# Kernel optimization log

Hardware: AMD Instinct MI355X
Metric: run time of the kernel (lower is better)

The kernel has to match this reference:

```python
import jax, jax.numpy as jnp
import numpy as np


def setup_inputs() -> dict:
    key = jax.random.key(0)
    k1, k2, k3, k4 = jax.random.split(key, 4)
    B, S, H = 1, 2048, 3072
    E, I = 4, 8192  # num_experts, intermediate_size
    x = jax.random.normal(k1, (B, S, H), dtype=jnp.float32)
    gate_w = jax.random.normal(k2, (E, H), dtype=jnp.float32) * 0.02
    w_gate_up = jax.random.normal(k3, (E, 2 * I, H), dtype=jnp.float32) * 0.02
    w_down = jax.random.normal(k4, (E, H, I), dtype=jnp.float32) * 0.02
    return {"x": x, "gate_w": gate_w, "w_gate_up": w_gate_up, "w_down": w_down, "top_k": 2}


def reference(x, gate_w, w_gate_up, w_down, top_k):
    # x: [B, S, H]; gate_w: [E, H]; w_gate_up: [E, 2I, H]; w_down: [E, H, I]
    B, S, H = x.shape
    E = gate_w.shape[0]
    # Gating: softmax over experts, then top-k values/indices
    logits = jnp.einsum('bsh,eh->bse', x, gate_w)
    probs = jax.nn.softmax(logits, axis=-1)
    gate_values, gate_indices = jax.lax.top_k(probs, top_k)  # [B, S, k]
    # Dense all-expert SwiGLU MLP (as in the original module)
    xf = x.reshape(-1, H)                                     # [N, H]
    up_states = jnp.einsum('nh,eih->nei', xf, w_gate_up)      # [N, E, 2I]
    gate, up = jnp.split(up_states, 2, axis=-1)               # [N, E, I] each
    hidden = up * jax.nn.silu(gate)                           # SwiGLU
    expert_out = jnp.einsum('nei,ehi->neh', hidden, w_down)   # [N, E, H]
    expert_out = expert_out.reshape(B, S, E, H)
    # Gather selected experts and combine with gate values
    sel = jnp.take_along_axis(expert_out, gate_indices[..., None], axis=2)  # [B, S, k, H]
    moe_output = jnp.sum(sel * gate_values[..., None], axis=2)              # [B, S, H]
    return moe_output
```

## Files before the change

kernel.cpp:

```cpp
#include <hip/hip_runtime.h>

#define S 2048
#define Hd 3072
#define NE 4
#define Id 8192
#define BK 64
#define RMAX 5120

typedef __attribute__((ext_vector_type(8))) short short8;
typedef __attribute__((ext_vector_type(4))) float f32x4;

__device__ __forceinline__ unsigned short f2bf(float f) {
    unsigned u = __builtin_bit_cast(unsigned, f);
    u += 0x7FFFu + ((u >> 16) & 1u);
    return (unsigned short)(u >> 16);
}

__device__ __forceinline__ void gload_lds16(const void* g, void* l) {
    __builtin_amdgcn_global_load_lds(
        (const __attribute__((address_space(1))) unsigned int*)g,
        (__attribute__((address_space(3))) unsigned int*)l,
        16, 0, 0);
}

#define BAR() __builtin_amdgcn_s_barrier();
#define LGKM0_SB() { asm volatile("s_waitcnt lgkmcnt(0)" ::: "memory"); __builtin_amdgcn_sched_barrier(0); }
#define VM6_SB()  { asm volatile("s_waitcnt vmcnt(6)" ::: "memory"); __builtin_amdgcn_sched_barrier(0); }

__global__ void gate_topk_kernel(const float* __restrict__ x,
                                 const float* __restrict__ gw,
                                 int* __restrict__ tok_e,
                                 float* __restrict__ tok_v) {
    const int t = blockIdx.x;
    const int lane = threadIdx.x & 63;
    const int wave = threadIdx.x >> 6;
    __shared__ float logits[NE];
    const float* xp = x + (size_t)t * Hd;
    const float* wp = gw + (size_t)wave * Hd;
    float s = 0.f;
    for (int h = lane; h < Hd; h += 64) s += xp[h] * wp[h];
#pragma unroll
    for (int o = 32; o > 0; o >>= 1) s += __shfl_xor(s, o);
    if (lane == 0) logits[wave] = s;
    __syncthreads();
    if (threadIdx.x == 0) {
        float m = logits[0];
#pragma unroll
        for (int e = 1; e < NE; e++) m = fmaxf(m, logits[e]);
        float p[NE]; float sum = 0.f;
#pragma unroll
        for (int e = 0; e < NE; e++) { p[e] = expf(logits[e] - m); sum += p[e]; }
        float inv = 1.f / sum;
#pragma unroll
        for (int e = 0; e < NE; e++) p[e] *= inv;
        int e0 = 0; float v0 = p[0];
#pragma unroll
        for (int e = 1; e < NE; e++) if (p[e] > v0) { e0 = e; v0 = p[e]; }
        int e1 = -1; float v1 = -1.f;
#pragma unroll
        for (int e = 0; e < NE; e++) if (e != e0 && p[e] > v1) { e1 = e; v1 = p[e]; }
        tok_e[t * 2] = e0; tok_e[t * 2 + 1] = e1;
        tok_v[t * 2] = v0; tok_v[t * 2 + 1] = v1;
    }
}

__global__ void route_kernel(const int* __restrict__ tok_e, const float* __restrict__ tok_v,
                             int* __restrict__ row_token, float* __restrict__ row_gate,
                             int* __restrict__ offsets) {
    __shared__ int cnt[NE], cur[NE], offs[NE + 1];
    const int tid = threadIdx.x;
    if (tid < NE) { cnt[tid] = 0; cur[tid] = 0; }
    __syncthreads();
    for (int i = tid; i < S * 2; i += 256) atomicAdd(&cnt[tok_e[i]], 1);
    __syncthreads();
    if (tid == 0) {
        int o = 0;
        for (int e = 0; e < NE; e++) { offs[e] = o; o += (cnt[e] + 255) / 256 * 256; }
        offs[NE] = o;
        for (int e = 0; e <= NE; e++) offsets[e] = offs[e];
    }
    __syncthreads();
    for (int r = tid; r < RMAX; r += 256) { row_token[r] = 0; row_gate[r] = 0.f; }
    __syncthreads();
    for (int i = tid; i < S * 2; i += 256) {
        int e = tok_e[i];
        int pos = atomicAdd(&cur[e], 1);
        int r = offs[e] + pos;
        row_token[r] = i >> 1;
        row_gate[r] = tok_v[i];
    }
}

__global__ void cvt_bf16_kernel(const float* __restrict__ src,
                                unsigned short* __restrict__ dst, size_t n16) {
    size_t stride = (size_t)gridDim.x * blockDim.x;
    for (size_t i = (size_t)blockIdx.x * blockDim.x + threadIdx.x; i < n16; i += stride) {
        size_t b = i * 16;
        f32x4 a0 = *(const f32x4*)(src + b);
        f32x4 a1 = *(const f32x4*)(src + b + 4);
        f32x4 a2 = *(const f32x4*)(src + b + 8);
        f32x4 a3 = *(const f32x4*)(src + b + 12);
        union { unsigned short u[8]; short8 v; } o0, o1;
#pragma unroll
        for (int j = 0; j < 4; j++) {
            o0.u[j] = f2bf(a0[j]); o0.u[4 + j] = f2bf(a1[j]);
            o1.u[j] = f2bf(a2[j]); o1.u[4 + j] = f2bf(a3[j]);
        }
        *(short8*)(dst + b) = o0.v;
        *(short8*)(dst + b + 8) = o1.v;
    }
}


#define ST_A0(buf, k) { gload_lds16(aP[0] + (k), &Ald[buf][raD[0]][0]); gload_lds16(aP[1] + (k), &Ald[buf][raD[1]][0]); }
#define ST_A1(buf, k) { gload_lds16(aP[2] + (k), &Ald[buf][raD[2]][0]); gload_lds16(aP[3] + (k), &Ald[buf][raD[3]][0]); }
#define ST_B0(buf, k) { gload_lds16(bP[0] + (k), &Bld[buf][rbD[0]][0]); gload_lds16(bP[1] + (k), &Bld[buf][rbD[1]][0]); }
#define ST_B1(buf, k) { gload_lds16(bP[2] + (k), &Bld[buf][rbD[2]][0]); gload_lds16(bP[3] + (k), &Bld[buf][rbD[3]][0]); }

#define READ_AFL(b) _Pragma("unroll") for (int mi = 0; mi < 4; mi++) _Pragma("unroll") for (int kk = 0; kk < 2; kk++) { \
    int row = wm * 128 + mi * 16 + c16; int slot = ((kk << 2) + c4) ^ l7; \
    afL[mi][kk] = *(const short8*)&Ald[b][row][slot * 8]; }
#define READ_AFH(b) _Pragma("unroll") for (int mi = 0; mi < 4; mi++) _Pragma("unroll") for (int kk = 0; kk < 2; kk++) { \
    int row = wm * 128 + 64 + mi * 16 + c16; int slot = ((kk << 2) + c4) ^ l7; \
    afH[mi][kk] = *(const short8*)&Ald[b][row][slot * 8]; }
#define READ_BFL(b) _Pragma("unroll") for (int n = 0; n < 2; n++) _Pragma("unroll") for (int kk = 0; kk < 2; kk++) { \
    int row = wn * 64 + n * 16 + c16; int slot = ((kk << 2) + c4) ^ l7; \
    bfL[n][kk] = *(const short8*)&Bld[b][row][slot * 8]; }
#define READ_BFH(b) _Pragma("unroll") for (int n = 0; n < 2; n++) _Pragma("unroll") for (int kk = 0; kk < 2; kk++) { \
    int row = wn * 64 + 32 + n * 16 + c16; int slot = ((kk << 2) + c4) ^ l7; \
    bfH[n][kk] = *(const short8*)&Bld[b][row][slot * 8]; }

#define MFMA_Q(AF, BF, MO, NO) _Pragma("unroll") for (int mi = 0; mi < 4; mi++) \
    _Pragma("unroll") for (int n = 0; n < 2; n++) _Pragma("unroll") for (int kk = 0; kk < 2; kk++) \
        acc[mi + MO][n + NO] = __builtin_amdgcn_mfma_f32_16x16x32_bf16(AF[mi][kk], BF[n][kk], acc[mi + MO][n + NO], 0, 0, 0);

#define KTILE_BODY(bR, bW, kN, kNN) { \
    short8 afL[4][2], afH[4][2], bfL[2][2], bfH[2][2]; \
     \
    READ_AFL(bR); READ_BFL(bR); \
    ST_B1(bW, kN); \
    BAR(); LGKM0_SB(); \
    __builtin_amdgcn_s_setprio(1); MFMA_Q(afL, bfL, 0, 0); __builtin_amdgcn_s_setprio(0); \
    BAR(); \
     \
    READ_AFH(bR); \
    ST_A0(bR, kNN); \
    BAR(); LGKM0_SB(); \
    __builtin_amdgcn_s_setprio(1); MFMA_Q(afH, bfL, 4, 0); __builtin_amdgcn_s_setprio(0); \
    BAR(); \
     \
    READ_BFH(bR); \
    ST_B0(bR, kNN); \
    BAR(); LGKM0_SB(); \
    __builtin_amdgcn_s_setprio(1); MFMA_Q(afL, bfH, 0, 2); __builtin_amdgcn_s_setprio(0); \
    BAR(); \
     \
    ST_A1(bR, kNN); \
    BAR(); \
    __builtin_amdgcn_s_setprio(1); MFMA_Q(afH, bfH, 4, 2); __builtin_amdgcn_s_setprio(0); \
    VM6_SB(); BAR(); }

__global__ __launch_bounds__(512, 2)
void gemm1_8p_kernel(const unsigned short* __restrict__ xb,
                     const unsigned short* __restrict__ wgu_b,
                     const int* __restrict__ row_token,
                     const int* __restrict__ offsets,
                     unsigned short* __restrict__ hidden) {
    __shared__ unsigned short Ald[2][256][BK];
    __shared__ unsigned short Bld[2][256][BK];

    const int id = blockIdx.x;
    const int xcd = id & 7, jj = id >> 3;
    const int ct = xcd * 8 + jj / 20;
    const int rt = jj % 20;
    const int rbase = rt * 256;
    if (rbase >= offsets[4]) return;
    int e = 3;
    if (rbase < offsets[1]) e = 0;
    else if (rbase < offsets[2]) e = 1;
    else if (rbase < offsets[3]) e = 2;

    const int tid = threadIdx.x;
    const int l = tid & 63;
    const int w = tid >> 6;
    const int wm = w >> 2, wn = w & 3;
    const int lr = l >> 3;
    const int g8 = ((l & 7) ^ lr) << 3;
    const int c16 = l & 15, c4 = l >> 4, l7 = l & 7;

    const unsigned short* aP[4]; int raD[4];
    const unsigned short* bP[4]; int rbD[4];
#pragma unroll
    for (int j = 0; j < 4; j++) {
        int r0 = w * 8 + (j & 1) * 128 + (j >> 1) * 64;
        raD[j] = r0;
        int tok = row_token[rbase + r0 + lr];
        aP[j] = xb + (size_t)tok * Hd + g8;
        int rb0 = (w & 3) * 8 + (w >> 2) * 64 + (j & 1) * 128 + (j >> 1) * 32;
        rbD[j] = rb0;
        int brow = rb0 + lr;
        int f = brow >> 4;
        size_t wr = (size_t)e * (2 * Id) + (size_t)(f & 1) * Id
                  + (size_t)ct * 128 + ((f >> 1) << 4) + (brow & 15);
        bP[j] = wgu_b + wr * Hd + g8;
    }

    f32x4 acc[8][4];
#pragma unroll
    for (int mi = 0; mi < 8; mi++)
#pragma unroll
        for (int n = 0; n < 4; n++) acc[mi][n] = (f32x4)0.f;

    ST_A0(0, 0); ST_B0(0, 0); ST_A1(0, 0); ST_B1(0, 0);
    ST_A0(1, BK); ST_B0(1, BK); ST_A1(1, BK);
    VM6_SB(); BAR();

    const int nt = Hd / BK;
    for (int t = 0; t < nt; ++t) {
        const int bR = t & 1, bW = bR ^ 1;
        const int kN  = (t + 1 < nt ? t + 1 : nt - 1) * BK;
        const int kNN = (t + 2 < nt ? t + 2 : nt - 1) * BK;
        KTILE_BODY(bR, bW, kN, kNN);
    }
    asm volatile("s_waitcnt vmcnt(0)" ::: "memory");

#pragma unroll
    for (int mi = 0; mi < 8; mi++)
#pragma unroll
        for (int np = 0; np < 2; np++) {
            int col = ct * 128 + (wn * 2 + np) * 16 + c16;
#pragma unroll
            for (int q = 0; q < 4; q++) {
                int row = rbase + wm * 128 + mi * 16 + c4 * 4 + q;
                float gv = acc[mi][2 * np][q], uv = acc[mi][2 * np + 1][q];
                float h = uv * gv / (1.f + expf(-gv));
                hidden[(size_t)row * Id + col] = f2bf(h);
            }
        }
}

__global__ __launch_bounds__(512, 2)
void gemm2_8p_kernel(const unsigned short* __restrict__ hidden,
                     const unsigned short* __restrict__ wd_b,
                     const int* __restrict__ row_token,
                     const float* __restrict__ row_gate,
                     const int* __restrict__ offsets,
                     float* __restrict__ out) {
    __shared__ unsigned short Ald[2][256][BK];
    __shared__ unsigned short Bld[2][256][BK];

    const int rt = blockIdx.x, ct = blockIdx.y;
    const int rbase = rt * 256;
    if (rbase >= offsets[4]) return;
    int e = 3;
    if (rbase < offsets[1]) e = 0;
    else if (rbase < offsets[2]) e = 1;
    else if (rbase < offsets[3]) e = 2;

    const int tid = threadIdx.x;
    const int l = tid & 63;
    const int w = tid >> 6;
    const int wm = w >> 2, wn = w & 3;
    const int lr = l >> 3;
    const int g8 = ((l & 7) ^ lr) << 3;
    const int c16 = l & 15, c4 = l >> 4, l7 = l & 7;

    const unsigned short* aP[4]; int raD[4];
    const unsigned short* bP[4]; int rbD[4];
#pragma unroll
    for (int j = 0; j < 4; j++) {
        int r0 = w * 8 + (j & 1) * 128 + (j >> 1) * 64;
        raD[j] = r0;
        aP[j] = hidden + (size_t)(rbase + r0 + lr) * Id + g8;
        int rb0 = (w & 3) * 8 + (w >> 2) * 64 + (j & 1) * 128 + (j >> 1) * 32;
        rbD[j] = rb0;
        size_t wr = (size_t)e * Hd + (size_t)ct * 256 + rb0 + lr;
        bP[j] = wd_b + wr * Id + g8;
    }

    f32x4 acc[8][4];
#pragma unroll
    for (int mi = 0; mi < 8; mi++)
#pragma unroll
        for (int n = 0; n < 4; n++) acc[mi][n] = (f32x4)0.f;

    ST_A0(0, 0); ST_B0(0, 0); ST_A1(0, 0); ST_B1(0, 0);
    ST_A0(1, BK); ST_B0(1, BK); ST_A1(1, BK);
    VM6_SB(); BAR();

    const int nt = Id / BK;
    for (int t = 0; t < nt; ++t) {
        const int bR = t & 1, bW = bR ^ 1;
        const int kN  = (t + 1 < nt ? t + 1 : nt - 1) * BK;
        const int kNN = (t + 2 < nt ? t + 2 : nt - 1) * BK;
        KTILE_BODY(bR, bW, kN, kNN);
    }
    asm volatile("s_waitcnt vmcnt(0)" ::: "memory");

#pragma unroll
    for (int mi = 0; mi < 8; mi++)
#pragma unroll
        for (int n = 0; n < 4; n++) {
            int col = ct * 256 + wn * 64 + n * 16 + c16;
#pragma unroll
            for (int q = 0; q < 4; q++) {
                int r = rbase + wm * 128 + mi * 16 + c4 * 4 + q;
                int tok = row_token[r];
                float gv = row_gate[r];
                if (gv != 0.f)
                    atomicAdd(&out[(size_t)tok * Hd + col], gv * acc[mi][n][q]);
            }
        }
}


__global__ __launch_bounds__(256, 2)
void gemm1_f32_kernel(const unsigned short* __restrict__ xb,
                      const float* __restrict__ wgu,
                      const int* __restrict__ row_token,
                      const int* __restrict__ offsets,
                      unsigned short* __restrict__ hidden) {
    __shared__ unsigned short As[128][BK];
    __shared__ unsigned short Bg[128][BK];
    __shared__ unsigned short Bu[128][BK];

    const int rt = blockIdx.x, ct = blockIdx.y;
    const int rbase = rt * 128;
    if (rbase >= offsets[4]) return;
    int e = 3;
    if (rbase < offsets[1]) e = 0;
    else if (rbase < offsets[2]) e = 1;
    else if (rbase < offsets[3]) e = 2;

    const int tid = threadIdx.x;
    const int lane = tid & 63;
    const int wave = tid >> 6;
    const int wm = wave >> 1, wn = wave & 1;

    const unsigned short* asrc[4];
#pragma unroll
    for (int i2 = 0; i2 < 4; i2++) {
        int sgi = i2 * 4 + wave;
        int row = sgi * 8 + (lane >> 3);
        int g = (lane & 7) ^ (row & 7);
        int tok = row_token[rbase + row];
        asrc[i2] = xb + (size_t)tok * Hd + g * 8;
    }
    const int col = tid >> 1;
    const int half = tid & 1;
    const size_t grow = (size_t)e * (2 * Id) + (size_t)ct * 128 + col;
    const float* bsrc_g = wgu + grow * Hd + half * 32;
    const float* bsrc_u = wgu + (grow + (size_t)Id) * Hd + half * 32;
    const int csw = col & 7;

    f32x4 accg[4][4], accu[4][4];
#pragma unroll
    for (int m = 0; m < 4; m++)
#pragma unroll
        for (int n = 0; n < 4; n++) { accg[m][n] = (f32x4)0.f; accu[m][n] = (f32x4)0.f; }

    for (int k0 = 0; k0 < Hd; k0 += BK) {
        __syncthreads();
#pragma unroll
        for (int i2 = 0; i2 < 4; i2++) {
            int sgi = i2 * 4 + wave;
            gload_lds16(asrc[i2] + k0, &As[sgi * 8][0]);
        }
        {
            const float* pg = bsrc_g + k0;
            const float* pu = bsrc_u + k0;
            f32x4 vg[8], vu[8];
#pragma unroll
            for (int j = 0; j < 8; j++) vg[j] = *(const f32x4*)(pg + j * 4);
#pragma unroll
            for (int j = 0; j < 8; j++) vu[j] = *(const f32x4*)(pu + j * 4);
#pragma unroll
            for (int j = 0; j < 4; j++) {
                union { unsigned short u[8]; short8 v8; } wg_, wu_;
#pragma unroll
                for (int q = 0; q < 4; q++) {
                    wg_.u[q] = f2bf(vg[2 * j][q]); wg_.u[4 + q] = f2bf(vg[2 * j + 1][q]);
                    wu_.u[q] = f2bf(vu[2 * j][q]); wu_.u[4 + q] = f2bf(vu[2 * j + 1][q]);
                }
                int gs = (half * 4 + j) ^ csw;
                *(short8*)&Bg[col][gs * 8] = wg_.v8;
                *(short8*)&Bu[col][gs * 8] = wu_.v8;
            }
        }
        __syncthreads();
#pragma unroll
        for (int kk = 0; kk < 2; kk++) {
            short8 af[4], bgf[4], buf_[4];
#pragma unroll
            for (int m = 0; m < 4; m++) {
                int r = wm * 64 + m * 16 + (lane & 15);
                int slot = (kk * 4 + (lane >> 4)) ^ (r & 7);
                af[m] = *(const short8*)&As[r][slot * 8];
            }
#pragma unroll
            for (int n = 0; n < 4; n++) {
                int c = wn * 64 + n * 16 + (lane & 15);
                int slot = (kk * 4 + (lane >> 4)) ^ (c & 7);
                bgf[n] = *(const short8*)&Bg[c][slot * 8];
                buf_[n] = *(const short8*)&Bu[c][slot * 8];
            }
#pragma unroll
            for (int m = 0; m < 4; m++)
#pragma unroll
                for (int n = 0; n < 4; n++) {
                    accg[m][n] = __builtin_amdgcn_mfma_f32_16x16x32_bf16(af[m], bgf[n], accg[m][n], 0, 0, 0);
                    accu[m][n] = __builtin_amdgcn_mfma_f32_16x16x32_bf16(af[m], buf_[n], accu[m][n], 0, 0, 0);
                }
        }
    }
#pragma unroll
    for (int m = 0; m < 4; m++) {
#pragma unroll
        for (int n = 0; n < 4; n++) {
            int c = ct * 128 + wn * 64 + n * 16 + (lane & 15);
#pragma unroll
            for (int q = 0; q < 4; q++) {
                int r = rbase + wm * 64 + m * 16 + (lane >> 4) * 4 + q;
                float g = accg[m][n][q], u = accu[m][n][q];
                float hval = u * g / (1.f + expf(-g));
                hidden[(size_t)r * Id + c] = f2bf(hval);
            }
        }
    }
}

__global__ __launch_bounds__(256, 2)
void gemm2_f32_kernel(const unsigned short* __restrict__ hidden,
                      const float* __restrict__ wd,
                      const int* __restrict__ row_token,
                      const float* __restrict__ row_gate,
                      const int* __restrict__ offsets,
                      float* __restrict__ out) {
    __shared__ unsigned short As[128][BK];
    __shared__ unsigned short Bs[128][BK];

    const int rt = blockIdx.x, ct = blockIdx.y;
    const int rbase = rt * 128;
    if (rbase >= offsets[4]) return;
    int e = 3;
    if (rbase < offsets[1]) e = 0;
    else if (rbase < offsets[2]) e = 1;
    else if (rbase < offsets[3]) e = 2;

    const int tid = threadIdx.x;
    const int lane = tid & 63;
    const int wave = tid >> 6;
    const int wm = wave >> 1, wn = wave & 1;

    const unsigned short* asrc[4];
#pragma unroll
    for (int i2 = 0; i2 < 4; i2++) {
        int sgi = i2 * 4 + wave;
        int row = sgi * 8 + (lane >> 3);
        int g = (lane & 7) ^ (row & 7);
        asrc[i2] = hidden + (size_t)(rbase + row) * Id + g * 8;
    }
    const int col = tid >> 1;
    const int half = tid & 1;
    const float* bsrc = wd + ((size_t)e * Hd + (size_t)ct * 128 + col) * Id + half * 32;
    const int csw = col & 7;

    f32x4 acc[4][4];
#pragma unroll
    for (int m = 0; m < 4; m++)
#pragma unroll
        for (int n = 0; n < 4; n++) acc[m][n] = (f32x4)0.f;

    for (int k0 = 0; k0 < Id; k0 += BK) {
        __syncthreads();
#pragma unroll
        for (int i2 = 0; i2 < 4; i2++) {
            int sgi = i2 * 4 + wave;
            gload_lds16(asrc[i2] + k0, &As[sgi * 8][0]);
        }
        {
            const float* pb = bsrc + k0;
            f32x4 vb[8];
#pragma unroll
            for (int j = 0; j < 8; j++) vb[j] = *(const f32x4*)(pb + j * 4);
#pragma unroll
            for (int j = 0; j < 4; j++) {
                union { unsigned short u[8]; short8 v8; } wb_;
#pragma unroll
                for (int q = 0; q < 4; q++) {
                    wb_.u[q] = f2bf(vb[2 * j][q]); wb_.u[4 + q] = f2bf(vb[2 * j + 1][q]);
                }
                int gs = (half * 4 + j) ^ csw;
                *(short8*)&Bs[col][gs * 8] = wb_.v8;
            }
        }
        __syncthreads();
#pragma unroll
        for (int kk = 0; kk < 2; kk++) {
            short8 af[4], bf[4];
#pragma unroll
            for (int m = 0; m < 4; m++) {
                int r = wm * 64 + m * 16 + (lane & 15);
                int slot = (kk * 4 + (lane >> 4)) ^ (r & 7);
                af[m] = *(const short8*)&As[r][slot * 8];
            }
#pragma unroll
            for (int n = 0; n < 4; n++) {
                int c = wn * 64 + n * 16 + (lane & 15);
                int slot = (kk * 4 + (lane >> 4)) ^ (c & 7);
                bf[n] = *(const short8*)&Bs[c][slot * 8];
            }
#pragma unroll
            for (int m = 0; m < 4; m++)
#pragma unroll
                for (int n = 0; n < 4; n++)
                    acc[m][n] = __builtin_amdgcn_mfma_f32_16x16x32_bf16(af[m], bf[n], acc[m][n], 0, 0, 0);
        }
    }
#pragma unroll
    for (int m = 0; m < 4; m++) {
#pragma unroll
        for (int n = 0; n < 4; n++) {
            int c = ct * 128 + wn * 64 + n * 16 + (lane & 15);
#pragma unroll
            for (int q = 0; q < 4; q++) {
                int r = rbase + wm * 64 + m * 16 + (lane >> 4) * 4 + q;
                int tok = row_token[r];
                float gv = row_gate[r];
                if (gv != 0.f)
                    atomicAdd(&out[(size_t)tok * Hd + c], gv * acc[m][n][q]);
            }
        }
    }
}

extern "C" void kernel_launch(void* const* d_in, const int* in_sizes, int n_in,
                              void* d_out, int out_size, void* d_ws, size_t ws_size,
                              hipStream_t stream) {
    const float* x   = (const float*)d_in[0];
    const float* gw  = (const float*)d_in[1];
    const float* wgu = (const float*)d_in[2];
    const float* wd  = (const float*)d_in[3];
    float* out = (float*)d_out;

    const size_t n_wgu = (size_t)NE * 2 * Id * Hd;
    const size_t n_wd  = (size_t)NE * Hd * Id;

    char* ws = (char*)d_ws;
    size_t o = 0;
    auto alloc = [&](size_t bytes) { void* p = ws + o; o = (o + bytes + 255) & ~(size_t)255; return p; };
    unsigned short* xb      = (unsigned short*)alloc((size_t)S * Hd * 2);
    unsigned short* hidden  = (unsigned short*)alloc((size_t)RMAX * Id * 2);
    int*   row_token = (int*)alloc(RMAX * 4);
    float* row_gate  = (float*)alloc(RMAX * 4);
    int*   offsets   = (int*)alloc(8 * 4);
    int*   tok_e     = (int*)alloc(S * 2 * 4);
    float* tok_v     = (float*)alloc(S * 2 * 4);
    unsigned short* wgu_b = (unsigned short*)alloc(n_wgu * 2);
    unsigned short* wd_b  = (unsigned short*)alloc(n_wd * 2);
    const bool big = (ws_size >= o);

    hipMemsetAsync(d_out, 0, (size_t)S * Hd * 4, stream);
    gate_topk_kernel<<<S, 256, 0, stream>>>(x, gw, tok_e, tok_v);
    route_kernel<<<1, 256, 0, stream>>>(tok_e, tok_v, row_token, row_gate, offsets);
    cvt_bf16_kernel<<<1024, 256, 0, stream>>>(x, xb, (size_t)S * Hd / 16);

    if (big) {
        cvt_bf16_kernel<<<4096, 256, 0, stream>>>(wgu, wgu_b, n_wgu / 16);
        cvt_bf16_kernel<<<4096, 256, 0, stream>>>(wd, wd_b, n_wd / 16);
        gemm1_8p_kernel<<<1280, 512, 0, stream>>>(xb, wgu_b, row_token, offsets, hidden);
        gemm2_8p_kernel<<<dim3(RMAX / 256, Hd / 256), 512, 0, stream>>>(
            hidden, wd_b, row_token, row_gate, offsets, out);
    } else {
        gemm1_f32_kernel<<<dim3(RMAX / 128, Id / 128), 256, 0, stream>>>(
            xb, wgu, row_token, offsets, hidden);
        gemm2_f32_kernel<<<dim3(RMAX / 128, Hd / 128), 256, 0, stream>>>(
            hidden, wd, row_token, row_gate, offsets, out);
    }
}
```

Measured before the change: 1.196 ms.

## Fuse fp32-to-bf16 weight conversion into GEMM B-tile loads, drop separate cast passes

Removes the two standalone weight conversion kernels and has both expert GEMMs read fp32 weights directly. The weights go through registers, are converted to bf16, and are written to swizzled LDS, with the loads spread across the k-tile phases and new vmcnt waits. This avoids writing and re-reading the full bf16 weight copies. In exchange each block streams twice as many weight bytes and does the conversion arithmetic inside the main loop. Every row tile re-converts the same weights, and register pressure rises. gemm2 also gains an XCD-aware block remap to a 1D grid.

```diff
diff --git a/kernel.cpp b/kernel.cpp
--- a/kernel.cpp
+++ b/kernel.cpp
@@ -25,7 +25,7 @@
 
 #define BAR() __builtin_amdgcn_s_barrier();
 #define LGKM0_SB() { asm volatile("s_waitcnt lgkmcnt(0)" ::: "memory"); __builtin_amdgcn_sched_barrier(0); }
-#define VM6_SB()  { asm volatile("s_waitcnt vmcnt(6)" ::: "memory"); __builtin_amdgcn_sched_barrier(0); }
+#define VMC_SB(n) { asm volatile("s_waitcnt vmcnt(" #n ")" ::: "memory"); __builtin_amdgcn_sched_barrier(0); }
 
 __global__ void gate_topk_kernel(const float* __restrict__ x,
                                  const float* __restrict__ gw,
@@ -114,8 +114,6 @@
 
 #define ST_A0(buf, k) { gload_lds16(aP[0] + (k), &Ald[buf][raD[0]][0]); gload_lds16(aP[1] + (k), &Ald[buf][raD[1]][0]); }
 #define ST_A1(buf, k) { gload_lds16(aP[2] + (k), &Ald[buf][raD[2]][0]); gload_lds16(aP[3] + (k), &Ald[buf][raD[3]][0]); }
-#define ST_B0(buf, k) { gload_lds16(bP[0] + (k), &Bld[buf][rbD[0]][0]); gload_lds16(bP[1] + (k), &Bld[buf][rbD[1]][0]); }
-#define ST_B1(buf, k) { gload_lds16(bP[2] + (k), &Bld[buf][rbD[2]][0]); gload_lds16(bP[3] + (k), &Bld[buf][rbD[3]][0]); }
 
 #define READ_AFL(b) _Pragma("unroll") for (int mi = 0; mi < 4; mi++) _Pragma("unroll") for (int kk = 0; kk < 2; kk++) { \
     int row = wm * 128 + mi * 16 + c16; int slot = ((kk << 2) + c4) ^ l7; \
@@ -134,35 +132,54 @@
     _Pragma("unroll") for (int n = 0; n < 2; n++) _Pragma("unroll") for (int kk = 0; kk < 2; kk++) \
         acc[mi + MO][n + NO] = __builtin_amdgcn_mfma_f32_16x16x32_bf16(AF[mi][kk], BF[n][kk], acc[mi + MO][n + NO], 0, 0, 0);
 
+#define LOAD_B_HALF(h, k) { \
+    bv[4*(h)+0] = *(const f32x4*)(bsrc + (k) + 16*(h)); \
+    bv[4*(h)+1] = *(const f32x4*)(bsrc + (k) + 16*(h) + 4); \
+    bv[4*(h)+2] = *(const f32x4*)(bsrc + (k) + 16*(h) + 8); \
+    bv[4*(h)+3] = *(const f32x4*)(bsrc + (k) + 16*(h) + 12); }
+
+#define WRITE_B_HALF(buf, h) { \
+    union { unsigned short u[8]; short8 v8; } w0_, w1_; \
+    _Pragma("unroll") for (int q = 0; q < 4; q++) { \
+        w0_.u[q] = f2bf(bv[4*(h)+0][q]); w0_.u[4+q] = f2bf(bv[4*(h)+1][q]); \
+        w1_.u[q] = f2bf(bv[4*(h)+2][q]); w1_.u[4+q] = f2bf(bv[4*(h)+3][q]); } \
+    *(short8*)&Bld[buf][colB][(((halfB<<2) + 2*(h) + 0) ^ cswB) * 8] = w0_.v8; \
+    *(short8*)&Bld[buf][colB][(((halfB<<2) + 2*(h) + 1) ^ cswB) * 8] = w1_.v8; }
+
 #define KTILE_BODY(bR, bW, kN, kNN) { \
     short8 afL[4][2], afH[4][2], bfL[2][2], bfH[2][2]; \
      \
+    LOAD_B_HALF(0, kN); \
+    __builtin_amdgcn_sched_barrier(0); \
     READ_AFL(bR); READ_BFL(bR); \
-    ST_B1(bW, kN); \
     BAR(); LGKM0_SB(); \
     __builtin_amdgcn_s_setprio(1); MFMA_Q(afL, bfL, 0, 0); __builtin_amdgcn_s_setprio(0); \
     BAR(); \
      \
+    LOAD_B_HALF(1, kN); \
+    ST_A0(bR, kNN); \
+    __builtin_amdgcn_sched_barrier(0); \
     READ_AFH(bR); \
-    ST_A0(bR, kNN); \
     BAR(); LGKM0_SB(); \
     __builtin_amdgcn_s_setprio(1); MFMA_Q(afH, bfL, 4, 0); __builtin_amdgcn_s_setprio(0); \
     BAR(); \
      \
+    VMC_SB(6); \
+    WRITE_B_HALF(bW, 0); \
+    ST_A1(bR, kNN); \
     READ_BFH(bR); \
-    ST_B0(bR, kNN); \
     BAR(); LGKM0_SB(); \
     __builtin_amdgcn_s_setprio(1); MFMA_Q(afL, bfH, 0, 2); __builtin_amdgcn_s_setprio(0); \
     BAR(); \
      \
-    ST_A1(bR, kNN); \
-    BAR(); \
+    VMC_SB(4); \
+    WRITE_B_HALF(bW, 1); \
     __builtin_amdgcn_s_setprio(1); MFMA_Q(afH, bfH, 4, 2); __builtin_amdgcn_s_setprio(0); \
-    VM6_SB(); BAR(); }
+    LGKM0_SB(); BAR(); }
 
 __global__ __launch_bounds__(512, 2)
 void gemm1_8p_kernel(const unsigned short* __restrict__ xb,
-                     const unsigned short* __restrict__ wgu_b,
+                     const float* __restrict__ wgu,
                      const int* __restrict__ row_token,
                      const int* __restrict__ offsets,
                      unsigned short* __restrict__ hidden) {
@@ -189,31 +206,33 @@
     const int c16 = l & 15, c4 = l >> 4, l7 = l & 7;
 
     const unsigned short* aP[4]; int raD[4];
-    const unsigned short* bP[4]; int rbD[4];
 #pragma unroll
     for (int j = 0; j < 4; j++) {
         int r0 = w * 8 + (j & 1) * 128 + (j >> 1) * 64;
         raD[j] = r0;
         int tok = row_token[rbase + r0 + lr];
         aP[j] = xb + (size_t)tok * Hd + g8;
-        int rb0 = (w & 3) * 8 + (w >> 2) * 64 + (j & 1) * 128 + (j >> 1) * 32;
-        rbD[j] = rb0;
-        int brow = rb0 + lr;
-        int f = brow >> 4;
-        size_t wr = (size_t)e * (2 * Id) + (size_t)(f & 1) * Id
-                  + (size_t)ct * 128 + ((f >> 1) << 4) + (brow & 15);
-        bP[j] = wgu_b + wr * Hd + g8;
-    }
+    }
+    const int colB = tid >> 1, halfB = tid & 1, cswB = colB & 7;
+    const int fB = colB >> 4;
+    const size_t wrB = (size_t)e * (2 * Id) + (size_t)(fB & 1) * Id
+                     + (size_t)ct * 128 + ((fB >> 1) << 4) + (colB & 15);
+    const float* bsrc = wgu + wrB * Hd + halfB * 32;
 
     f32x4 acc[8][4];
 #pragma unroll
     for (int mi = 0; mi < 8; mi++)
 #pragma unroll
         for (int n = 0; n < 4; n++) acc[mi][n] = (f32x4)0.f;
-
-    ST_A0(0, 0); ST_B0(0, 0); ST_A1(0, 0); ST_B1(0, 0);
-    ST_A0(1, BK); ST_B0(1, BK); ST_A1(1, BK);
-    VM6_SB(); BAR();
+    f32x4 bv[8];
+
+    ST_A0(0, 0); ST_A1(0, 0);
+    LOAD_B_HALF(0, 0); LOAD_B_HALF(1, 0);
+    __builtin_amdgcn_sched_barrier(0);
+    ST_A0(1, BK); ST_A1(1, BK);
+    VMC_SB(4);
+    WRITE_B_HALF(0, 0); WRITE_B_HALF(0, 1);
+    LGKM0_SB(); BAR();
 
     const int nt = Hd / BK;
     for (int t = 0; t < nt; ++t) {
@@ -241,7 +260,7 @@
 
 __global__ __launch_bounds__(512, 2)
 void gemm2_8p_kernel(const unsigned short* __restrict__ hidden,
-                     const unsigned short* __restrict__ wd_b,
+                     const float* __restrict__ wd,
                      const int* __restrict__ row_token,
                      const float* __restrict__ row_gate,
                      const int* __restrict__ offsets,
@@ -249,7 +268,11 @@
     __shared__ unsigned short Ald[2][256][BK];
     __shared__ unsigned short Bld[2][256][BK];
 
-    const int rt = blockIdx.x, ct = blockIdx.y;
+    const int id = blockIdx.x;
+    const int xcd = id & 7, jj = id >> 3;
+    const int j12 = xcd * 30 + jj;
+    const int ct = j12 / 20;
+    const int rt = j12 % 20;
     const int rbase = rt * 256;
     if (rbase >= offsets[4]) return;
     int e = 3;
@@ -266,27 +289,29 @@
     const int c16 = l & 15, c4 = l >> 4, l7 = l & 7;
 
     const unsigned short* aP[4]; int raD[4];
-    const unsigned short* bP[4]; int rbD[4];
 #pragma unroll
     for (int j = 0; j < 4; j++) {
         int r0 = w * 8 + (j & 1) * 128 + (j >> 1) * 64;
         raD[j] = r0;
         aP[j] = hidden + (size_t)(rbase + r0 + lr) * Id + g8;
-        int rb0 = (w & 3) * 8 + (w >> 2) * 64 + (j & 1) * 128 + (j >> 1) * 32;
-        rbD[j] = rb0;
-        size_t wr = (size_t)e * Hd + (size_t)ct * 256 + rb0 + lr;
-        bP[j] = wd_b + wr * Id + g8;
-    }
+    }
+    const int colB = tid >> 1, halfB = tid & 1, cswB = colB & 7;
+    const float* bsrc = wd + ((size_t)e * Hd + (size_t)ct * 256 + colB) * Id + halfB * 32;
 
     f32x4 acc[8][4];
 #pragma unroll
     for (int mi = 0; mi < 8; mi++)
 #pragma unroll
         for (int n = 0; n < 4; n++) acc[mi][n] = (f32x4)0.f;
-
-    ST_A0(0, 0); ST_B0(0, 0); ST_A1(0, 0); ST_B1(0, 0);
-    ST_A0(1, BK); ST_B0(1, BK); ST_A1(1, BK);
-    VM6_SB(); BAR();
+    f32x4 bv[8];
+
+    ST_A0(0, 0); ST_A1(0, 0);
+    LOAD_B_HALF(0, 0); LOAD_B_HALF(1, 0);
+    __builtin_amdgcn_sched_barrier(0);
+    ST_A0(1, BK); ST_A1(1, BK);
+    VMC_SB(4);
+    WRITE_B_HALF(0, 0); WRITE_B_HALF(0, 1);
+    LGKM0_SB(); BAR();
 
     const int nt = Id / BK;
     for (int t = 0; t < nt; ++t) {
@@ -542,9 +567,6 @@
     const float* wgu = (const float*)d_in[2];
     const float* wd  = (const float*)d_in[3];
     float* out = (float*)d_out;
-
-    const size_t n_wgu = (size_t)NE * 2 * Id * Hd;
-    const size_t n_wd  = (size_t)NE * Hd * Id;
 
     char* ws = (char*)d_ws;
     size_t o = 0;
@@ -556,8 +578,6 @@
     int*   offsets   = (int*)alloc(8 * 4);
     int*   tok_e     = (int*)alloc(S * 2 * 4);
     float* tok_v     = (float*)alloc(S * 2 * 4);
-    unsigned short* wgu_b = (unsigned short*)alloc(n_wgu * 2);
-    unsigned short* wd_b  = (unsigned short*)alloc(n_wd * 2);
     const bool big = (ws_size >= o);
 
     hipMemsetAsync(d_out, 0, (size_t)S * Hd * 4, stream);
@@ -566,11 +586,8 @@
     cvt_bf16_kernel<<<1024, 256, 0, stream>>>(x, xb, (size_t)S * Hd / 16);
 
     if (big) {
-        cvt_bf16_kernel<<<4096, 256, 0, stream>>>(wgu, wgu_b, n_wgu / 16);
-        cvt_bf16_kernel<<<4096, 256, 0, stream>>>(wd, wd_b, n_wd / 16);
-        gemm1_8p_kernel<<<1280, 512, 0, stream>>>(xb, wgu_b, row_token, offsets, hidden);
-        gemm2_8p_kernel<<<dim3(RMAX / 256, Hd / 256), 512, 0, stream>>>(
-            hidden, wd_b, row_token, row_gate, offsets, out);
+        gemm1_8p_kernel<<<1280, 512, 0, stream>>>(xb, wgu, row_token, offsets, hidden);
+        gemm2_8p_kernel<<<240, 512, 0, stream>>>(hidden, wd, row_token, row_gate, offsets, out);
     } else {
         gemm1_f32_kernel<<<dim3(RMAX / 128, Id / 128), 256, 0, stream>>>(
             xb, wgu, row_token, offsets, hidden);
```

New measurement: 2.111 ms. 76.5% more time.

## Fuse gating and conversions into one prologue, overlap down-weight conversion with GEMM1

Applied to the files above, without the earlier changes.

Merges the gate/top-k kernel, the activation bf16 conversion and the gate_up weight conversion into a single launch that splits its blocks across the three jobs. The down-projection weight conversion moves into the first GEMM launch as extra leading blocks, so it can run alongside GEMM1 tiles instead of as a separate serial kernel. The goal is to cut launch gaps and let bandwidth-bound conversion share the device with compute. In exchange, GEMM1 blocks now compete with conversion blocks for CUs and memory bandwidth, and the block-count split is hand-tuned.

```diff
diff --git a/kernel.cpp b/kernel.cpp
--- a/kernel.cpp
+++ b/kernel.cpp
@@ -7,6 +7,11 @@
 #define BK 64
 #define RMAX 5120
 
+#define CVT1_BLKS 3072
+#define CVTX_BLKS 128
+#define GATE_BLKS 2048
+#define CVTW_BLKS 256
+
 typedef __attribute__((ext_vector_type(8))) short short8;
 typedef __attribute__((ext_vector_type(4))) float f32x4;
 
@@ -26,6 +31,77 @@
 #define BAR() __builtin_amdgcn_s_barrier();
 #define LGKM0_SB() { asm volatile("s_waitcnt lgkmcnt(0)" ::: "memory"); __builtin_amdgcn_sched_barrier(0); }
 #define VM6_SB()  { asm volatile("s_waitcnt vmcnt(6)" ::: "memory"); __builtin_amdgcn_sched_barrier(0); }
+
+__device__ __forceinline__ void cvt_range(const float* __restrict__ src,
+                                          unsigned short* __restrict__ dst,
+                                          size_t n16, int bid, int nblk, int nthr) {
+    size_t stride = (size_t)nblk * nthr;
+    for (size_t i = (size_t)bid * nthr + threadIdx.x; i < n16; i += stride) {
+        size_t b = i * 16;
+        f32x4 a0 = *(const f32x4*)(src + b);
+        f32x4 a1 = *(const f32x4*)(src + b + 4);
+        f32x4 a2 = *(const f32x4*)(src + b + 8);
+        f32x4 a3 = *(const f32x4*)(src + b + 12);
+        union { unsigned short u[8]; short8 v; } o0, o1;
+#pragma unroll
+        for (int j = 0; j < 4; j++) {
+            o0.u[j] = f2bf(a0[j]); o0.u[4 + j] = f2bf(a1[j]);
+            o1.u[j] = f2bf(a2[j]); o1.u[4 + j] = f2bf(a3[j]);
+        }
+        *(short8*)(dst + b) = o0.v;
+        *(short8*)(dst + b + 8) = o1.v;
+    }
+}
+
+__global__ __launch_bounds__(256)
+void fused_pre_kernel(const float* __restrict__ x,
+                      const float* __restrict__ gw,
+                      const float* __restrict__ wgu,
+                      unsigned short* __restrict__ wgu_b,
+                      unsigned short* __restrict__ xb,
+                      int* __restrict__ tok_e,
+                      float* __restrict__ tok_v) {
+    const int bid = blockIdx.x;
+    if (bid < CVT1_BLKS) {
+        cvt_range(wgu, wgu_b, (size_t)NE * 2 * Id * Hd / 16, bid, CVT1_BLKS, 256);
+        return;
+    }
+    if (bid < CVT1_BLKS + CVTX_BLKS) {
+        cvt_range(x, xb, (size_t)S * Hd / 16, bid - CVT1_BLKS, CVTX_BLKS, 256);
+        return;
+    }
+    const int t = bid - CVT1_BLKS - CVTX_BLKS;
+    const int lane = threadIdx.x & 63;
+    const int wave = threadIdx.x >> 6;
+    __shared__ float logits[NE];
+    const float* xp = x + (size_t)t * Hd;
+    const float* wp = gw + (size_t)wave * Hd;
+    float s = 0.f;
+    for (int h = lane; h < Hd; h += 64) s += xp[h] * wp[h];
+#pragma unroll
+    for (int o = 32; o > 0; o >>= 1) s += __shfl_xor(s, o);
+    if (lane == 0) logits[wave] = s;
+    __syncthreads();
+    if (threadIdx.x == 0) {
+        float m = logits[0];
+#pragma unroll
+        for (int e = 1; e < NE; e++) m = fmaxf(m, logits[e]);
+        float p[NE]; float sum = 0.f;
+#pragma unroll
+        for (int e = 0; e < NE; e++) { p[e] = expf(logits[e] - m); sum += p[e]; }
+        float inv = 1.f / sum;
+#pragma unroll
+        for (int e = 0; e < NE; e++) p[e] *= inv;
+        int e0 = 0; float v0 = p[0];
+#pragma unroll
+        for (int e = 1; e < NE; e++) if (p[e] > v0) { e0 = e; v0 = p[e]; }
+        int e1 = -1; float v1 = -1.f;
+#pragma unroll
+        for (int e = 0; e < NE; e++) if (e != e0 && p[e] > v1) { e1 = e; v1 = p[e]; }
+        tok_e[t * 2] = e0; tok_e[t * 2 + 1] = e1;
+        tok_v[t * 2] = v0; tok_v[t * 2 + 1] = v1;
+    }
+}
 
 __global__ void gate_topk_kernel(const float* __restrict__ x,
                                  const float* __restrict__ gw,
@@ -93,22 +169,7 @@
 
 __global__ void cvt_bf16_kernel(const float* __restrict__ src,
                                 unsigned short* __restrict__ dst, size_t n16) {
-    size_t stride = (size_t)gridDim.x * blockDim.x;
-    for (size_t i = (size_t)blockIdx.x * blockDim.x + threadIdx.x; i < n16; i += stride) {
-        size_t b = i * 16;
-        f32x4 a0 = *(const f32x4*)(src + b);
-        f32x4 a1 = *(const f32x4*)(src + b + 4);
-        f32x4 a2 = *(const f32x4*)(src + b + 8);
-        f32x4 a3 = *(const f32x4*)(src + b + 12);
-        union { unsigned short u[8]; short8 v; } o0, o1;
-#pragma unroll
-        for (int j = 0; j < 4; j++) {
-            o0.u[j] = f2bf(a0[j]); o0.u[4 + j] = f2bf(a1[j]);
-            o1.u[j] = f2bf(a2[j]); o1.u[4 + j] = f2bf(a3[j]);
-        }
-        *(short8*)(dst + b) = o0.v;
-        *(short8*)(dst + b + 8) = o1.v;
-    }
+    cvt_range(src, dst, n16, blockIdx.x, gridDim.x, blockDim.x);
 }
 
 
@@ -163,13 +224,19 @@
 __global__ __launch_bounds__(512, 2)
 void gemm1_8p_kernel(const unsigned short* __restrict__ xb,
                      const unsigned short* __restrict__ wgu_b,
+                     const float* __restrict__ wd,
+                     unsigned short* __restrict__ wd_b,
                      const int* __restrict__ row_token,
                      const int* __restrict__ offsets,
                      unsigned short* __restrict__ hidden) {
     __shared__ unsigned short Ald[2][256][BK];
     __shared__ unsigned short Bld[2][256][BK];
 
-    const int id = blockIdx.x;
+    if (blockIdx.x < CVTW_BLKS) {
+        cvt_range(wd, wd_b, (size_t)NE * Hd * Id / 16, blockIdx.x, CVTW_BLKS, 512);
+        return;
+    }
+    const int id = blockIdx.x - CVTW_BLKS;
     const int xcd = id & 7, jj = id >> 3;
     const int ct = xcd * 8 + jj / 20;
     const int rt = jj % 20;
@@ -561,17 +628,19 @@
     const bool big = (ws_size >= o);
 
     hipMemsetAsync(d_out, 0, (size_t)S * Hd * 4, stream);
-    gate_topk_kernel<<<S, 256, 0, stream>>>(x, gw, tok_e, tok_v);
-    route_kernel<<<1, 256, 0, stream>>>(tok_e, tok_v, row_token, row_gate, offsets);
-    cvt_bf16_kernel<<<1024, 256, 0, stream>>>(x, xb, (size_t)S * Hd / 16);
 
     if (big) {
-        cvt_bf16_kernel<<<4096, 256, 0, stream>>>(wgu, wgu_b, n_wgu / 16);
-        cvt_bf16_kernel<<<4096, 256, 0, stream>>>(wd, wd_b, n_wd / 16);
-        gemm1_8p_kernel<<<1280, 512, 0, stream>>>(xb, wgu_b, row_token, offsets, hidden);
+        fused_pre_kernel<<<CVT1_BLKS + CVTX_BLKS + GATE_BLKS, 256, 0, stream>>>(
+            x, gw, wgu, wgu_b, xb, tok_e, tok_v);
+        route_kernel<<<1, 256, 0, stream>>>(tok_e, tok_v, row_token, row_gate, offsets);
+        gemm1_8p_kernel<<<CVTW_BLKS + 1280, 512, 0, stream>>>(
+            xb, wgu_b, wd, wd_b, row_token, offsets, hidden);
         gemm2_8p_kernel<<<dim3(RMAX / 256, Hd / 256), 512, 0, stream>>>(
             hidden, wd_b, row_token, row_gate, offsets, out);
     } else {
+        gate_topk_kernel<<<S, 256, 0, stream>>>(x, gw, tok_e, tok_v);
+        route_kernel<<<1, 256, 0, stream>>>(tok_e, tok_v, row_token, row_gate, offsets);
+        cvt_bf16_kernel<<<1024, 256, 0, stream>>>(x, xb, (size_t)S * Hd / 16);
         gemm1_f32_kernel<<<dim3(RMAX / 128, Id / 128), 256, 0, stream>>>(
             xb, wgu, row_token, offsets, hidden);
         gemm2_f32_kernel<<<dim3(RMAX / 128, Hd / 128), 256, 0, stream>>>(
```

Measured after the change: 1.180 ms. About the same (-1.4%).
